# Kernel tuning notes

Hardware: AMD Instinct MI355X
Metric: run time of the kernel (lower is better)

## Reference

```python
import jax, jax.numpy as jnp
import numpy as np

NUM_CODES = 8192
EMBED_DIM = 256
N_TOKENS = 65536
COMMITMENT_COST = 0.25


def setup_inputs() -> dict:
    key = jax.random.key(0)
    k1, k2 = jax.random.split(key)
    inputs = jax.random.normal(k1, (N_TOKENS, EMBED_DIM), dtype=jnp.float32)
    # torch init: uniform(-1/num_codes, 1/num_codes); use normal-scale equivalent via uniform
    weight = jax.random.uniform(k2, (NUM_CODES, EMBED_DIM), dtype=jnp.float32,
                                minval=-1.0 / NUM_CODES, maxval=1.0 / NUM_CODES)
    return {"inputs": inputs, "weight": weight}


def reference(inputs, weight):
    inputs_sq = jnp.sum(inputs * inputs, axis=1, keepdims=True)      # (N, 1)
    embed_sq = jnp.sum(weight * weight, axis=1)                      # (K,)
    distances = inputs_sq + embed_sq - 2.0 * (inputs @ weight.T)     # (N, K)
    indices = jnp.argmin(distances, axis=1)                          # (N,)
    quantized = jnp.take(weight, indices, axis=0)                    # (N, D)

    codebook_loss = jnp.mean((quantized - jax.lax.stop_gradient(inputs)) ** 2)
    commit_loss = jnp.mean((inputs - jax.lax.stop_gradient(quantized)) ** 2)
    vq_loss = codebook_loss + COMMITMENT_COST * commit_loss

    # straight-through estimator
    quantized_st = inputs + jax.lax.stop_gradient(quantized - inputs)
    return quantized_st, indices, vq_loss, codebook_loss, commit_loss
```

## Files before the change

### kernel.cpp

```cpp
#include <hip/hip_runtime.h>

#define N_TOK  65536
#define N_CODE 8192
#define DIM    256

typedef _Float16 f16;
typedef _Float16 f16x8 __attribute__((ext_vector_type(8)));
typedef float    f32x4 __attribute__((ext_vector_type(4)));

__global__ __launch_bounds__(256) void rowsq_kernel(const float* __restrict__ src,
                                                    float* __restrict__ dst, int nrows) {
    int row  = blockIdx.x * 4 + (threadIdx.x >> 6);
    int lane = threadIdx.x & 63;
    if (row >= nrows) return;
    float4 v = ((const float4*)(src + (size_t)row * DIM))[lane];
    float s = v.x * v.x + v.y * v.y + v.z * v.z + v.w * v.w;
#pragma unroll
    for (int off = 32; off; off >>= 1) s += __shfl_down(s, off, 64);
    if (lane == 0) dst[row] = s;
}

__global__ __launch_bounds__(256) void splitw_kernel(const float* __restrict__ W,
                                                     f16* __restrict__ W1,
                                                     f16* __restrict__ W2) {
    int f = blockIdx.x * 256 + threadIdx.x;
    float4 v = ((const float4*)W)[f];
    union { f16 h[4]; uint2 u; } p1, p2;
    float e[4] = {v.x, v.y, v.z, v.w};
#pragma unroll
    for (int i = 0; i < 4; ++i) {
        float ws = e[i] * 16384.0f;
        f16 w1 = (f16)ws;
        float r = (ws - (float)w1) * 2048.0f;
        p1.h[i] = w1; p2.h[i] = (f16)r;
    }
    ((uint2*)W1)[f] = p1.u;
    ((uint2*)W2)[f] = p2.u;
}

__global__ __launch_bounds__(256, 2) void argmin_mfma4(
    const float* __restrict__ X, const f16* __restrict__ W1, const f16* __restrict__ W2,
    const float* __restrict__ sxq, const float* __restrict__ esq,
    int* __restrict__ out_idx) {

    __shared__ char wbuf[65536];

    const int tid  = threadIdx.x;
    const int lane = tid & 63;
    const int wv   = tid >> 6;
    const int cl   = lane & 15;
    const int q    = lane >> 4;
    const int wavetok0 = blockIdx.x * 128 + wv * 32;

    f16x8 a1[2][8], a2[2][8];
#pragma unroll
    for (int mt = 0; mt < 2; ++mt)
#pragma unroll
        for (int s = 0; s < 8; ++s) {
            const float* p = X + (size_t)(wavetok0 + mt * 16 + cl) * DIM + s * 32 + q * 8;
            float4 v0 = ((const float4*)p)[0];
            float4 v1 = ((const float4*)p)[1];
            float e[8] = {v0.x, v0.y, v0.z, v0.w, v1.x, v1.y, v1.z, v1.w};
#pragma unroll
            for (int j = 0; j < 8; ++j) {
                f16 h = (f16)e[j];
                float r = (e[j] - (float)h) * 2048.0f;
                a1[mt][s][j] = h;
                a2[mt][s][j] = (f16)r;
            }
        }

    float sxr[8];
#pragma unroll
    for (int mt = 0; mt < 2; ++mt)
#pragma unroll
        for (int r = 0; r < 4; ++r)
            sxr[mt * 4 + r] = sxq[wavetok0 + mt * 16 + q * 4 + r];

    float bestd[8];
    int   besti[8];
#pragma unroll
    for (int i = 0; i < 8; ++i) { bestd[i] = 3.4e38f; besti[i] = 0x7fffffff; }

    auto stage = [&](int ct2, int sel) {
#pragma unroll
        for (int t = 0; t < 8; ++t) {
            int fi = wv * 8 + t;
            int L  = fi >> 4;
            int cp = fi & 15;
            int c  = 2 * cp + (lane >> 5);
            int o  = (lane & 31) ^ (c & 7);
            const f16* gsrc = (L ? W2 : W1) + (size_t)(ct2 * 32 + c) * DIM + o * 8;
            char* ldst = wbuf + sel * 32768 + L * 16384 + cp * 1024;
            __builtin_amdgcn_global_load_lds(
                (const __attribute__((address_space(1))) unsigned int*)gsrc,
                (__attribute__((address_space(3))) unsigned int*)ldst, 16, 0, 0);
        }
    };

    stage(0, 0);
    __syncthreads();

    for (int ct = 0; ct < N_CODE / 32; ++ct) {
        if (ct + 1 < N_CODE / 32) stage(ct + 1, (ct + 1) & 1);

        float se0 = esq[ct * 32 + cl];
        float se1 = esq[ct * 32 + 16 + cl];

        f32x4 mainA[2][2], cross[2][2];
#pragma unroll
        for (int mt = 0; mt < 2; ++mt)
#pragma unroll
            for (int nt = 0; nt < 2; ++nt) {
                mainA[mt][nt] = (f32x4){0.f, 0.f, 0.f, 0.f};
                cross[mt][nt] = (f32x4){0.f, 0.f, 0.f, 0.f};
            }

        const char* base = wbuf + (ct & 1) * 32768;
#pragma unroll
        for (int s = 0; s < 8; ++s) {
            f16x8 b1[2], b2[2];
#pragma unroll
            for (int nt = 0; nt < 2; ++nt) {
                int off = ((nt * 16 + cl) * 32 + (((s * 4 + q) ^ (cl & 7)))) * 16;
                b1[nt] = *(const f16x8*)(base + off);
                b2[nt] = *(const f16x8*)(base + 16384 + off);
            }
            __builtin_amdgcn_s_setprio(1);
#pragma unroll
            for (int mt = 0; mt < 2; ++mt)
#pragma unroll
                for (int nt = 0; nt < 2; ++nt) {
                    mainA[mt][nt] = __builtin_amdgcn_mfma_f32_16x16x32_f16(a1[mt][s], b1[nt], mainA[mt][nt], 0, 0, 0);
                    cross[mt][nt] = __builtin_amdgcn_mfma_f32_16x16x32_f16(a2[mt][s], b1[nt], cross[mt][nt], 0, 0, 0);
                    cross[mt][nt] = __builtin_amdgcn_mfma_f32_16x16x32_f16(a1[mt][s], b2[nt], cross[mt][nt], 0, 0, 0);
                }
            __builtin_amdgcn_s_setprio(0);
        }

#pragma unroll
        for (int mt = 0; mt < 2; ++mt)
#pragma unroll
            for (int nt = 0; nt < 2; ++nt)
#pragma unroll
                for (int r = 0; r < 4; ++r) {
                    float mc = fmaf(cross[mt][nt][r], 4.8828125e-4f, mainA[mt][nt][r]);
                    float t1 = sxr[mt * 4 + r] + (nt ? se1 : se0);
                    float d  = fmaf(-1.220703125e-4f, mc, t1);
                    int slot = mt * 4 + r;
                    if (d < bestd[slot]) {
                        bestd[slot] = d;
                        besti[slot] = ct * 32 + nt * 16 + cl;
                    }
                }
        __syncthreads();
    }

#pragma unroll
    for (int slot = 0; slot < 8; ++slot) {
        float d = bestd[slot];
        int   i = besti[slot];
#pragma unroll
        for (int off = 1; off < 16; off <<= 1) {
            float od = __shfl_xor(d, off, 64);
            int   oi = __shfl_xor(i, off, 64);
            if (od < d || (od == d && oi < i)) { d = od; i = oi; }
        }
        if (cl == 0)
            out_idx[wavetok0 + (slot >> 2) * 16 + q * 4 + (slot & 3)] = i;
    }
}

__global__ __launch_bounds__(256) void finalize_kernel(
    const float* __restrict__ X, const float* __restrict__ W,
    const int* __restrict__ idx, float* __restrict__ outQ,
    float* __restrict__ outI, double* __restrict__ accum) {
    __shared__ double wsum[4];
    int wid  = threadIdx.x >> 6;
    int lane = threadIdx.x & 63;
    int token = blockIdx.x * 4 + wid;
    int id = idx[token];
    float4 x = ((const float4*)(X + (size_t)token * DIM))[lane];
    float4 qv = ((const float4*)(W + (size_t)id * DIM))[lane];
    float4 o;
    o.x = x.x + (qv.x - x.x);
    o.y = x.y + (qv.y - x.y);
    o.z = x.z + (qv.z - x.z);
    o.w = x.w + (qv.w - x.w);
    ((float4*)(outQ + (size_t)token * DIM))[lane] = o;
    float dx = x.x - qv.x, dy = x.y - qv.y, dz = x.z - qv.z, dw = x.w - qv.w;
    float s = dx * dx + dy * dy + dz * dz + dw * dw;
#pragma unroll
    for (int off = 32; off; off >>= 1) s += __shfl_down(s, off, 64);
    if (lane == 0) {
        outI[token] = (float)id;
        wsum[wid] = (double)s;
    }
    __syncthreads();
    if (threadIdx.x == 0) {
        double t = wsum[0] + wsum[1] + wsum[2] + wsum[3];
        atomicAdd(&accum[blockIdx.x & 127], t);
    }
}

__global__ void scalars_kernel(const double* __restrict__ accum, float* __restrict__ out) {
    double mse = 0.0;
    for (int i = 0; i < 128; ++i) mse += accum[i];
    mse /= (double)((size_t)N_TOK * DIM);
    float c = (float)mse;
    out[0] = c + 0.25f * c;
    out[1] = c;
    out[2] = c;
}

extern "C" void kernel_launch(void* const* d_in, const int* in_sizes, int n_in,
                              void* d_out, int out_size, void* d_ws, size_t ws_size,
                              hipStream_t stream) {
    const float* X = (const float*)d_in[0];
    const float* W = (const float*)d_in[1];

    float* outQ = (float*)d_out;
    float* outI = outQ + (size_t)N_TOK * DIM;
    float* outS = outI + N_TOK;

    char* ws = (char*)d_ws;
    double* accum = (double*)ws;
    float* esq = (float*)(ws + 4096);
    float* sxq = (float*)(ws + 4096 + 32768);
    int*   idx = (int*)(ws + 4096 + 32768 + 262144);
    f16*   W1  = (f16*)(ws + (1 << 20));
    f16*   W2  = (f16*)(ws + (1 << 20) + 4194304);

    hipMemsetAsync(accum, 0, 128 * sizeof(double), stream);
    splitw_kernel<<<N_CODE * DIM / 4 / 256, 256, 0, stream>>>(W, W1, W2);
    rowsq_kernel<<<N_CODE / 4, 256, 0, stream>>>(W, esq, N_CODE);
    rowsq_kernel<<<N_TOK / 4, 256, 0, stream>>>(X, sxq, N_TOK);
    argmin_mfma4<<<N_TOK / 128, 256, 0, stream>>>(X, W1, W2, sxq, esq, idx);
    finalize_kernel<<<N_TOK / 4, 256, 0, stream>>>(X, W, idx, outQ, outI, accum);
    scalars_kernel<<<1, 1, 0, stream>>>(accum, outS);
}
```

Measured before the change: 754.1 us.

## Switch argmin distance GEMM from 16x16x32 to 32x32x16 MFMA tiles

```diff
diff --git a/kernel.cpp b/kernel.cpp
--- a/kernel.cpp
+++ b/kernel.cpp
@@ -6,7 +6,7 @@
 
 typedef _Float16 f16;
 typedef _Float16 f16x8 __attribute__((ext_vector_type(8)));
-typedef float    f32x4 __attribute__((ext_vector_type(4)));
+typedef float    f32x16 __attribute__((ext_vector_type(16)));
 
 __global__ __launch_bounds__(256) void rowsq_kernel(const float* __restrict__ src,
                                                     float* __restrict__ dst, int nrows) {
@@ -38,7 +38,7 @@
     ((uint2*)W2)[f] = p2.u;
 }
 
-__global__ __launch_bounds__(256, 2) void argmin_mfma4(
+__global__ __launch_bounds__(256, 2) void argmin_mfma6(
     const float* __restrict__ X, const f16* __restrict__ W1, const f16* __restrict__ W2,
     const float* __restrict__ sxq, const float* __restrict__ esq,
     int* __restrict__ out_idx) {
@@ -48,39 +48,35 @@
     const int tid  = threadIdx.x;
     const int lane = tid & 63;
     const int wv   = tid >> 6;
-    const int cl   = lane & 15;
-    const int q    = lane >> 4;
+    const int col  = lane & 31;
+    const int hi   = lane >> 5;
     const int wavetok0 = blockIdx.x * 128 + wv * 32;
 
-    f16x8 a1[2][8], a2[2][8];
-#pragma unroll
-    for (int mt = 0; mt < 2; ++mt)
-#pragma unroll
-        for (int s = 0; s < 8; ++s) {
-            const float* p = X + (size_t)(wavetok0 + mt * 16 + cl) * DIM + s * 32 + q * 8;
-            float4 v0 = ((const float4*)p)[0];
-            float4 v1 = ((const float4*)p)[1];
-            float e[8] = {v0.x, v0.y, v0.z, v0.w, v1.x, v1.y, v1.z, v1.w};
-#pragma unroll
-            for (int j = 0; j < 8; ++j) {
-                f16 h = (f16)e[j];
-                float r = (e[j] - (float)h) * 2048.0f;
-                a1[mt][s][j] = h;
-                a2[mt][s][j] = (f16)r;
-            }
-        }
-
-    float sxr[8];
-#pragma unroll
-    for (int mt = 0; mt < 2; ++mt)
-#pragma unroll
-        for (int r = 0; r < 4; ++r)
-            sxr[mt * 4 + r] = sxq[wavetok0 + mt * 16 + q * 4 + r];
-
-    float bestd[8];
-    int   besti[8];
-#pragma unroll
-    for (int i = 0; i < 8; ++i) { bestd[i] = 3.4e38f; besti[i] = 0x7fffffff; }
+    f16x8 a1[16], a2[16];
+#pragma unroll
+    for (int ks = 0; ks < 16; ++ks) {
+        const float* p = X + (size_t)(wavetok0 + col) * DIM + ks * 16 + hi * 8;
+        float4 v0 = ((const float4*)p)[0];
+        float4 v1 = ((const float4*)p)[1];
+        float e[8] = {v0.x, v0.y, v0.z, v0.w, v1.x, v1.y, v1.z, v1.w};
+#pragma unroll
+        for (int j = 0; j < 8; ++j) {
+            f16 h = (f16)e[j];
+            float r = (e[j] - (float)h) * 2048.0f;
+            a1[ks][j] = h;
+            a2[ks][j] = (f16)r;
+        }
+    }
+
+    float sxr[16];
+#pragma unroll
+    for (int r = 0; r < 16; ++r)
+        sxr[r] = sxq[wavetok0 + (r & 3) + 8 * (r >> 2) + 4 * hi];
+
+    float bestd[16];
+    int   besti[16];
+#pragma unroll
+    for (int i = 0; i < 16; ++i) { bestd[i] = 3.4e38f; besti[i] = 0x7fffffff; }
 
     auto stage = [&](int ct2, int sel) {
 #pragma unroll
@@ -101,73 +97,55 @@
     stage(0, 0);
     __syncthreads();
 
+    const int x7 = col & 7;
+
     for (int ct = 0; ct < N_CODE / 32; ++ct) {
         if (ct + 1 < N_CODE / 32) stage(ct + 1, (ct + 1) & 1);
 
-        float se0 = esq[ct * 32 + cl];
-        float se1 = esq[ct * 32 + 16 + cl];
-
-        f32x4 mainA[2][2], cross[2][2];
-#pragma unroll
-        for (int mt = 0; mt < 2; ++mt)
-#pragma unroll
-            for (int nt = 0; nt < 2; ++nt) {
-                mainA[mt][nt] = (f32x4){0.f, 0.f, 0.f, 0.f};
-                cross[mt][nt] = (f32x4){0.f, 0.f, 0.f, 0.f};
+        float se = esq[ct * 32 + col];
+
+        f32x16 mainA, cross;
+#pragma unroll
+        for (int r = 0; r < 16; ++r) { mainA[r] = 0.f; cross[r] = 0.f; }
+
+        const char* lbase = wbuf + (ct & 1) * 32768 + col * 512;
+#pragma unroll
+        for (int ks = 0; ks < 16; ++ks) {
+            int perm = ((ks * 2 + hi) ^ x7) << 4;
+            f16x8 b1 = *(const f16x8*)(lbase + perm);
+            f16x8 b2 = *(const f16x8*)(lbase + 16384 + perm);
+            __builtin_amdgcn_s_setprio(1);
+            mainA = __builtin_amdgcn_mfma_f32_32x32x16_f16(a1[ks], b1, mainA, 0, 0, 0);
+            cross = __builtin_amdgcn_mfma_f32_32x32x16_f16(a2[ks], b1, cross, 0, 0, 0);
+            cross = __builtin_amdgcn_mfma_f32_32x32x16_f16(a1[ks], b2, cross, 0, 0, 0);
+            __builtin_amdgcn_s_setprio(0);
+        }
+
+#pragma unroll
+        for (int r = 0; r < 16; ++r) {
+            float mc = fmaf(cross[r], 4.8828125e-4f, mainA[r]);
+            float t1 = sxr[r] + se;
+            float d  = fmaf(-1.220703125e-4f, mc, t1);
+            if (d < bestd[r]) {
+                bestd[r] = d;
+                besti[r] = ct * 32 + col;
             }
-
-        const char* base = wbuf + (ct & 1) * 32768;
-#pragma unroll
-        for (int s = 0; s < 8; ++s) {
-            f16x8 b1[2], b2[2];
-#pragma unroll
-            for (int nt = 0; nt < 2; ++nt) {
-                int off = ((nt * 16 + cl) * 32 + (((s * 4 + q) ^ (cl & 7)))) * 16;
-                b1[nt] = *(const f16x8*)(base + off);
-                b2[nt] = *(const f16x8*)(base + 16384 + off);
-            }
-            __builtin_amdgcn_s_setprio(1);
-#pragma unroll
-            for (int mt = 0; mt < 2; ++mt)
-#pragma unroll
-                for (int nt = 0; nt < 2; ++nt) {
-                    mainA[mt][nt] = __builtin_amdgcn_mfma_f32_16x16x32_f16(a1[mt][s], b1[nt], mainA[mt][nt], 0, 0, 0);
-                    cross[mt][nt] = __builtin_amdgcn_mfma_f32_16x16x32_f16(a2[mt][s], b1[nt], cross[mt][nt], 0, 0, 0);
-                    cross[mt][nt] = __builtin_amdgcn_mfma_f32_16x16x32_f16(a1[mt][s], b2[nt], cross[mt][nt], 0, 0, 0);
-                }
-            __builtin_amdgcn_s_setprio(0);
-        }
-
-#pragma unroll
-        for (int mt = 0; mt < 2; ++mt)
-#pragma unroll
-            for (int nt = 0; nt < 2; ++nt)
-#pragma unroll
-                for (int r = 0; r < 4; ++r) {
-                    float mc = fmaf(cross[mt][nt][r], 4.8828125e-4f, mainA[mt][nt][r]);
-                    float t1 = sxr[mt * 4 + r] + (nt ? se1 : se0);
-                    float d  = fmaf(-1.220703125e-4f, mc, t1);
-                    int slot = mt * 4 + r;
-                    if (d < bestd[slot]) {
-                        bestd[slot] = d;
-                        besti[slot] = ct * 32 + nt * 16 + cl;
-                    }
-                }
+        }
         __syncthreads();
     }
 
 #pragma unroll
-    for (int slot = 0; slot < 8; ++slot) {
-        float d = bestd[slot];
-        int   i = besti[slot];
-#pragma unroll
-        for (int off = 1; off < 16; off <<= 1) {
+    for (int r = 0; r < 16; ++r) {
+        float d = bestd[r];
+        int   i = besti[r];
+#pragma unroll
+        for (int off = 1; off < 32; off <<= 1) {
             float od = __shfl_xor(d, off, 64);
             int   oi = __shfl_xor(i, off, 64);
             if (od < d || (od == d && oi < i)) { d = od; i = oi; }
         }
-        if (cl == 0)
-            out_idx[wavetok0 + (slot >> 2) * 16 + q * 4 + (slot & 3)] = i;
+        if (col == 0)
+            out_idx[wavetok0 + (r & 3) + 8 * (r >> 2) + 4 * hi] = i;
     }
 }
 
@@ -235,7 +213,7 @@
     splitw_kernel<<<N_CODE * DIM / 4 / 256, 256, 0, stream>>>(W, W1, W2);
     rowsq_kernel<<<N_CODE / 4, 256, 0, stream>>>(W, esq, N_CODE);
     rowsq_kernel<<<N_TOK / 4, 256, 0, stream>>>(X, sxq, N_TOK);
-    argmin_mfma4<<<N_TOK / 128, 256, 0, stream>>>(X, W1, W2, sxq, esq, idx);
+    argmin_mfma6<<<N_TOK / 128, 256, 0, stream>>>(X, W1, W2, sxq, esq, idx);
     finalize_kernel<<<N_TOK / 4, 256, 0, stream>>>(X, W, idx, outQ, outI, accum);
     scalars_kernel<<<1, 1, 0, stream>>>(accum, outS);
 }
```

New measurement: 960.9 us. 27.4% more time.
